# Kernel tuning notes

Hardware: AMD Instinct MI355X
Metric: run time of the kernel (lower is better)

## Reference

```python
import math
import jax, jax.numpy as jnp
import numpy as np

B, T, C, H, E, K = 2, 2048, 1024, 16, 8, 2
HID = 4 * C
D = C // H

def new_gelu(x):
    return 0.5 * x * (1.0 + jnp.tanh(math.sqrt(2.0 / math.pi) * (x + 0.044715 * x ** 3)))

def layer_norm(x, g, b, eps=1e-5):
    mu = jnp.mean(x, axis=-1, keepdims=True)
    var = jnp.var(x, axis=-1, keepdims=True)
    return (x - mu) / jnp.sqrt(var + eps) * g + b

def setup_inputs():
    key = jax.random.key(0)
    ks = jax.random.split(key, 8)
    s = 0.02
    return {
        'x': jax.random.normal(ks[0], (B, T, C), jnp.float32),
        'ln1_g': jnp.ones((C,), jnp.float32), 'ln1_b': jnp.zeros((C,), jnp.float32),
        'ln2_g': jnp.ones((C,), jnp.float32), 'ln2_b': jnp.zeros((C,), jnp.float32),
        'attn_w': (jax.random.normal(ks[1], (C, 3 * C), jnp.float32) * s),
        'attn_b': jnp.zeros((3 * C,), jnp.float32),
        'proj_w': (jax.random.normal(ks[2], (C, C), jnp.float32) * s),
        'proj_b': jnp.zeros((C,), jnp.float32),
        'router_w': (jax.random.normal(ks[3], (C, E), jnp.float32) * s),
        'fc_w': (jax.random.normal(ks[4], (E, C, HID), jnp.float32) * s),
        'fc_b': jnp.zeros((E, HID), jnp.float32),
        'pj_w': (jax.random.normal(ks[5], (E, HID, C), jnp.float32) * s),
        'pj_b': jnp.zeros((E, C), jnp.float32),
    }

def reference(x, ln1_g, ln1_b, ln2_g, ln2_b, attn_w, attn_b, proj_w, proj_b, router_w, fc_w, fc_b, pj_w, pj_b):
    # --- causal self-attention with residual ---
    h = layer_norm(x, ln1_g, ln1_b)
    qkv = h @ attn_w + attn_b                              # [B,T,3C]
    q, k, v = jnp.split(qkv, 3, axis=-1)
    q = q.reshape(B, T, H, D).transpose(0, 2, 1, 3)        # [B,H,T,D]
    k = k.reshape(B, T, H, D).transpose(0, 2, 1, 3)
    v = v.reshape(B, T, H, D).transpose(0, 2, 1, 3)
    att = jnp.einsum('bhqd,bhkd->bhqk', q, k) * (1.0 / math.sqrt(D))
    mask = jnp.tril(jnp.ones((T, T), dtype=bool))
    att = jnp.where(mask, att, jnp.float32(-jnp.inf))
    att = jax.nn.softmax(att, axis=-1)                     # dropout p=0 (eval)
    y = jnp.einsum('bhqk,bhkd->bhqd', att, v)
    y = y.transpose(0, 2, 1, 3).reshape(B, T, C)
    x = x + (y @ proj_w + proj_b)
    # --- MoE FFN with residual ---
    h2 = layer_norm(x, ln2_g, ln2_b).reshape(B * T, C)     # [N,C]
    logits = h2 @ router_w                                 # [N,E]
    probs = jax.nn.softmax(logits, axis=-1)
    topk_p, topk_i = jax.lax.top_k(probs, K)               # [N,K]
    topk_p = topk_p / jnp.sum(topk_p, axis=-1, keepdims=True)
    # dense combine weights: zero outside selected experts (same math as scatter)
    gate = jnp.zeros((B * T, E), h2.dtype).at[jnp.arange(B * T)[:, None], topk_i].add(topk_p)
    out = jnp.zeros_like(h2)
    for e in range(E):  # fixed small expert loop
        he = new_gelu(h2 @ fc_w[e] + fc_b[e])              # [N,HID]
        out = out + gate[:, e:e + 1] * (he @ pj_w[e] + pj_b[e])
    return x + out.reshape(B, T, C)
```

## Files before the change

kernel.cpp:

```cpp
#include <hip/hip_runtime.h>
#include <math.h>


typedef __bf16 b16v8 __attribute__((ext_vector_type(8)));
typedef float f32x4 __attribute__((ext_vector_type(4)));

#define MFMA(a, b, c) __builtin_amdgcn_mfma_f32_16x16x32_bf16(a, b, c, 0, 0, 0)

#define GLOAD_LDS16(g, l)                                          \
  __builtin_amdgcn_global_load_lds(                                \
      (const __attribute__((address_space(1))) void*)(g),          \
      (__attribute__((address_space(3))) void*)(l), 16, 0, 0)

constexpr int Bc = 2, Tc = 2048, Cc = 1024, Hc = 16, Dc = 64;
constexpr int Nc = Bc * Tc;
constexpr int HIDc = 4096;
constexpr int Ec = 8;
constexpr int NPAIR = Nc * 2;
constexpr int NRBMAX = NPAIR / 128 + Ec;
constexpr float LOG2E = 1.4426950408889634f;

__device__ inline unsigned short f32_bf16(float f) {
  union { float f; unsigned u; } x; x.f = f;
  unsigned r = x.u + 0x7fffu + ((x.u >> 16) & 1u);
  return (unsigned short)(r >> 16);
}

__device__ inline float gelu_f(float x) {
  float t = 2.3021188f * x * (1.f + 0.044715f * x * x);
  float e = __builtin_amdgcn_exp2f(-t);
  return x * __builtin_amdgcn_rcpf(1.f + e);
}

__device__ inline int swz(int row, int g) {
  return row * 64 + ((g ^ (row & 7)) * 8);
}

__global__ __launch_bounds__(256) void convT_kernel(
    const float* __restrict__ src, unsigned short* __restrict__ dst,
    int K, int N) {
  const size_t sb = (size_t)blockIdx.z * K * N;
  const int n0 = blockIdx.x * 32, k0 = blockIdx.y * 32;
  __shared__ float t[32][33];
  const int tx = threadIdx.x & 31, ty = threadIdx.x >> 5;
#pragma unroll
  for (int j = 0; j < 4; ++j)
    t[ty + j * 8][tx] = src[sb + (size_t)(k0 + ty + j * 8) * N + n0 + tx];
  __syncthreads();
#pragma unroll
  for (int j = 0; j < 4; ++j)
    dst[sb + (size_t)(n0 + ty + j * 8) * K + k0 + tx] = f32_bf16(t[tx][ty + j * 8]);
}

__global__ __launch_bounds__(256) void ln1_kernel(
    const float* __restrict__ x, const float* __restrict__ g,
    const float* __restrict__ b, unsigned short* __restrict__ out) {
  const int row = blockIdx.x;
  const int tid = threadIdx.x;
  const float* xr = x + (size_t)row * Cc;
  float v[4]; float s = 0.f, q = 0.f;
#pragma unroll
  for (int j = 0; j < 4; ++j) { v[j] = xr[tid + j * 256]; s += v[j]; q += v[j] * v[j]; }
#pragma unroll
  for (int m = 1; m <= 32; m <<= 1) { s += __shfl_xor(s, m); q += __shfl_xor(q, m); }
  __shared__ float red[2][4];
  const int w = tid >> 6;
  if ((tid & 63) == 0) { red[0][w] = s; red[1][w] = q; }
  __syncthreads();
  s = red[0][0] + red[0][1] + red[0][2] + red[0][3];
  q = red[1][0] + red[1][1] + red[1][2] + red[1][3];
  const float mean = s * (1.f / Cc);
  const float var = q * (1.f / Cc) - mean * mean;
  const float rstd = rsqrtf(var + 1e-5f);
#pragma unroll
  for (int j = 0; j < 4; ++j) {
    int c = tid + j * 256;
    out[(size_t)row * Cc + c] = f32_bf16((v[j] - mean) * rstd * g[c] + b[c]);
  }
}

__global__ __launch_bounds__(256) void ln2_router_kernel(
    const float* __restrict__ x, const float* __restrict__ g,
    const float* __restrict__ b, const float* __restrict__ rw,
    unsigned short* __restrict__ out, int* __restrict__ tki, float* __restrict__ tkp) {
  const int row = blockIdx.x;
  const int tid = threadIdx.x;
  const float* xr = x + (size_t)row * Cc;
  float v[4]; float s = 0.f, q = 0.f;
#pragma unroll
  for (int j = 0; j < 4; ++j) { v[j] = xr[tid + j * 256]; s += v[j]; q += v[j] * v[j]; }
#pragma unroll
  for (int m = 1; m <= 32; m <<= 1) { s += __shfl_xor(s, m); q += __shfl_xor(q, m); }
  __shared__ float red[2][4];
  const int w = tid >> 6;
  if ((tid & 63) == 0) { red[0][w] = s; red[1][w] = q; }
  __syncthreads();
  s = red[0][0] + red[0][1] + red[0][2] + red[0][3];
  q = red[1][0] + red[1][1] + red[1][2] + red[1][3];
  const float mean = s * (1.f / Cc);
  const float var = q * (1.f / Cc) - mean * mean;
  const float rstd = rsqrtf(var + 1e-5f);
  float lg[8] = {0.f, 0.f, 0.f, 0.f, 0.f, 0.f, 0.f, 0.f};
#pragma unroll
  for (int j = 0; j < 4; ++j) {
    int c = tid + j * 256;
    float nv = (v[j] - mean) * rstd * g[c] + b[c];
    out[(size_t)row * Cc + c] = f32_bf16(nv);
    const float* rwc = rw + c * 8;
#pragma unroll
    for (int e = 0; e < 8; ++e) lg[e] += nv * rwc[e];
  }
#pragma unroll
  for (int m = 1; m <= 32; m <<= 1) {
#pragma unroll
    for (int e = 0; e < 8; ++e) lg[e] += __shfl_xor(lg[e], m);
  }
  __shared__ float rl[4][8];
  if ((tid & 63) == 0) {
#pragma unroll
    for (int e = 0; e < 8; ++e) rl[w][e] = lg[e];
  }
  __syncthreads();
  if (tid == 0) {
    float L[8];
#pragma unroll
    for (int e = 0; e < 8; ++e) L[e] = rl[0][e] + rl[1][e] + rl[2][e] + rl[3][e];
    int i1 = 0;
    for (int e = 1; e < 8; ++e) if (L[e] > L[i1]) i1 = e;
    int i2 = (i1 == 0) ? 1 : 0;
    for (int e = 0; e < 8; ++e) if (e != i1 && L[e] > L[i2]) i2 = e;
    float e2 = expf(L[i2] - L[i1]);
    float inv = 1.f / (1.f + e2);
    tki[row * 2] = i1; tki[row * 2 + 1] = i2;
    tkp[row * 2] = inv; tkp[row * 2 + 1] = e2 * inv;
  }
}

__global__ __launch_bounds__(256) void count_kernel(
    const int* __restrict__ tki, int* __restrict__ counts) {
  int n = blockIdx.x * 256 + threadIdx.x;
  if (n >= Nc) return;
  atomicAdd(&counts[tki[n * 2]], 1);
  atomicAdd(&counts[tki[n * 2 + 1]], 1);
}

__global__ void scan_kernel(const int* __restrict__ counts,
                            int* __restrict__ eoff, int* __restrict__ cursor,
                            int* __restrict__ tbl_e, int* __restrict__ tbl_r0,
                            int* __restrict__ tbl_n) {
  if (threadIdx.x == 0 && blockIdx.x == 0) {
    int s = 0, nb = 0;
    for (int e = 0; e < Ec; ++e) {
      eoff[e] = s; cursor[e] = s;
      for (int r = 0; r < counts[e]; r += 128) {
        tbl_e[nb] = e; tbl_r0[nb] = r; ++nb;
      }
      s += counts[e];
    }
    eoff[Ec] = s;
    *tbl_n = nb;
  }
}

__global__ __launch_bounds__(256) void assign_kernel(
    const int* __restrict__ tki, int* __restrict__ cursor,
    int* __restrict__ slot_tok, int* __restrict__ tok2slot) {
  int n = blockIdx.x * 256 + threadIdx.x;
  if (n >= Nc) return;
#pragma unroll
  for (int kk = 0; kk < 2; ++kk) {
    int e = tki[n * 2 + kk];
    int slot = atomicAdd(&cursor[e], 1);
    slot_tok[slot] = n;
    tok2slot[n * 2 + kk] = slot;
  }
}

struct GArgs {
  const unsigned short* A;
  const unsigned short* Bt;
  const float* bias;
  int M, N, K, lda, ldb, klen;
  size_t Bstride; int biasStride;
  const int* eoff;
  const int* slot_tok;
  const int* tbl_e;
  const int* tbl_r0;
  const int* tbl_n;
  float* outF;
  const float* resid;
  unsigned short* outB;
  unsigned short* outK;
  unsigned short* outV;
};

template <int MODE>
__global__ __launch_bounds__(256) void gemm128b(GArgs g) {
  int e = 0, s0 = 0, Meff = g.M, row0;
  if constexpr (MODE == 2 || MODE == 3) {
    if ((int)blockIdx.y >= *g.tbl_n) return;
    e = g.tbl_e[blockIdx.y];
    row0 = g.tbl_r0[blockIdx.y];
    s0 = g.eoff[e];
    Meff = g.eoff[e + 1] - s0;
  } else {
    row0 = blockIdx.y * 128;
  }
  const int kh = (MODE == 3) ? blockIdx.z : 0;
  const int col0 = blockIdx.x * 128;
  const int kbase = kh * g.klen;

  __shared__ __align__(16) unsigned short As[128 * 64];
  __shared__ __align__(16) unsigned short Bs[128 * 64];

  const int tid = threadIdx.x;
  const int lane = tid & 63, w = tid >> 6;
  const int wr = w >> 1, wc = w & 1;
  const int fr = lane & 15, fg = lane >> 4;

  const unsigned short* Bt = g.Bt + (size_t)e * g.Bstride;
  const float* bias = g.bias + (size_t)e * g.biasStride;

  size_t aaddr[4], baddr[4];
#pragma unroll
  for (int i = 0; i < 4; ++i) {
    int pos = i * 256 + tid;
    int r = pos >> 3;
    int c8 = ((pos & 7) ^ (r & 7)) * 8;
    int gr = row0 + r;
    if (gr >= Meff) gr = Meff - 1;
    int srcrow;
    if constexpr (MODE == 2) srcrow = g.slot_tok[s0 + gr];
    else if constexpr (MODE == 3) srcrow = s0 + gr;
    else srcrow = gr;
    aaddr[i] = (size_t)srcrow * g.lda + kbase + c8;
    baddr[i] = (size_t)(col0 + r) * g.ldb + kbase + c8;
  }

  auto STAGE = [&](int k0) {
#pragma unroll
    for (int i = 0; i < 4; ++i) {
      GLOAD_LDS16(g.A + aaddr[i] + k0, &As[i * 2048 + w * 512]);
      GLOAD_LDS16(Bt + baddr[i] + k0, &Bs[i * 2048 + w * 512]);
    }
  };

  f32x4 acc[4][4] = {};
  const int nt = g.klen / 64;

  for (int t = 0; t < nt; ++t) {
    if (t) __syncthreads();
    STAGE(t * 64);
    __syncthreads();
    b16v8 af[4][2], bf_[4][2];
#pragma unroll
    for (int mi = 0; mi < 4; ++mi) {
      const int ar = wr * 64 + mi * 16 + fr;
      af[mi][0] = *(const b16v8*)&As[swz(ar, fg)];
      af[mi][1] = *(const b16v8*)&As[swz(ar, 4 + fg)];
    }
#pragma unroll
    for (int ni = 0; ni < 4; ++ni) {
      const int br = wc * 64 + ni * 16 + fr;
      bf_[ni][0] = *(const b16v8*)&Bs[swz(br, fg)];
      bf_[ni][1] = *(const b16v8*)&Bs[swz(br, 4 + fg)];
    }
#pragma unroll
    for (int mi = 0; mi < 4; ++mi)
#pragma unroll
      for (int ni = 0; ni < 4; ++ni) {
        acc[mi][ni] = MFMA(af[mi][0], bf_[ni][0], acc[mi][ni]);
        acc[mi][ni] = MFMA(af[mi][1], bf_[ni][1], acc[mi][ni]);
      }
  }

  float* outF3 = nullptr;
  if constexpr (MODE == 3) outF3 = g.outF + (size_t)kh * NPAIR * Cc;

#pragma unroll
  for (int mi = 0; mi < 4; ++mi) {
#pragma unroll
    for (int ni = 0; ni < 4; ++ni) {
#pragma unroll
      for (int rr = 0; rr < 4; ++rr) {
        int row = row0 + wr * 64 + mi * 16 + fg * 4 + rr;
        int col = col0 + wc * 64 + ni * 16 + fr;
        if (row >= Meff) continue;
        float bval = bias[col];
        if constexpr (MODE == 3) { if (kh != 0) bval = 0.f; }
        float val = acc[mi][ni][rr] + bval;
        if constexpr (MODE == 0) {
          int bb = row >> 11, tt = row & (Tc - 1);
          int which = col >> 10, cj = col & (Cc - 1);
          int hd = cj >> 6, d = cj & 63;
          if (which == 0)
            g.outB[(((size_t)(bb * Hc + hd)) * Tc + tt) * Dc + d] = f32_bf16(val);
          else if (which == 1)
            g.outK[(((size_t)(bb * Hc + hd)) * Tc + tt) * Dc + d] = f32_bf16(val);
          else
            g.outV[(((size_t)(bb * Hc + hd)) * Dc + d) * Tc + tt] = f32_bf16(val);
        } else if constexpr (MODE == 1) {
          size_t o = (size_t)row * g.N + col;
          g.outF[o] = val + g.resid[o];
        } else if constexpr (MODE == 2) {
          g.outB[(size_t)(s0 + row) * g.N + col] = f32_bf16(gelu_f(val));
        } else {
          outF3[(size_t)(s0 + row) * g.N + col] = val;
        }
      }
    }
  }
}

__global__ __launch_bounds__(512) void attn_kernel(
    const unsigned short* __restrict__ q, const unsigned short* __restrict__ k,
    const unsigned short* __restrict__ v, unsigned short* __restrict__ y) {
  const int qt = blockIdx.x, bh = blockIdx.y;
  const int qbase = qt * 128;
  __shared__ __align__(16) unsigned short ldsK[64][72];
  __shared__ __align__(16) unsigned short ldsVT[64][72];
  __shared__ __align__(16) unsigned short ldsP[8][16][72];
  const int tid = threadIdx.x, lane = tid & 63, w = tid >> 6;
  const int fr = lane & 15, fg = lane >> 4;
  const size_t base = (size_t)bh * Tc * Dc;
  const int qrow = qbase + w * 16 + fr;
  b16v8 qa0 = *(const b16v8*)(q + base + (size_t)qrow * Dc + fg * 8);
  b16v8 qa1 = *(const b16v8*)(q + base + (size_t)qrow * Dc + 32 + fg * 8);
  float m[4], lsum[4] = {0.f, 0.f, 0.f, 0.f};
#pragma unroll
  for (int r = 0; r < 4; ++r) m[r] = -3.0e38f;
  f32x4 oacc[4] = {};
  constexpr float SC = 0.125f * LOG2E;

  const int sr = tid >> 3, scb = (tid & 7) * 8;
  const int ntile = (qbase + 128) / 64;

  *(uint4*)&ldsK[sr][scb]  = *(const uint4*)(k + base + (size_t)sr * Dc + scb);
  *(uint4*)&ldsVT[sr][scb] = *(const uint4*)(v + base + (size_t)sr * Tc + scb);
  __syncthreads();

  for (int ti = 0; ti < ntile; ++ti) {
    const int kb = ti * 64;
    uint4 kreg, vreg;
    const bool more = (ti + 1 < ntile);
    if (more) {
      const int kn = kb + 64;
      kreg = *(const uint4*)(k + base + (size_t)(kn + sr) * Dc + scb);
      vreg = *(const uint4*)(v + base + (size_t)sr * Tc + kn + scb);
    }

    f32x4 s[4];
#pragma unroll
    for (int ni = 0; ni < 4; ++ni) {
      b16v8 kb0 = *(const b16v8*)&ldsK[ni * 16 + fr][fg * 8];
      b16v8 kb1 = *(const b16v8*)&ldsK[ni * 16 + fr][32 + fg * 8];
      f32x4 z = {};
      z = MFMA(qa0, kb0, z);
      z = MFMA(qa1, kb1, z);
      s[ni] = z;
    }
    const bool diag = (kb + 64 > qbase + w * 16);
#pragma unroll
    for (int ni = 0; ni < 4; ++ni) {
#pragma unroll
      for (int r = 0; r < 4; ++r) {
        float sv = s[ni][r] * SC;
        if (diag) {
          int gq = qbase + w * 16 + fg * 4 + r;
          int kv = kb + ni * 16 + fr;
          if (kv > gq) sv = -3.0e38f;
        }
        s[ni][r] = sv;
      }
    }
#pragma unroll
    for (int r = 0; r < 4; ++r) {
      float mx = fmaxf(fmaxf(s[0][r], s[1][r]), fmaxf(s[2][r], s[3][r]));
#pragma unroll
      for (int msk = 1; msk <= 8; msk <<= 1) mx = fmaxf(mx, __shfl_xor(mx, msk));
      float mnew = fmaxf(m[r], mx);
      float alpha = __builtin_amdgcn_exp2f(m[r] - mnew);
      float psum = 0.f;
#pragma unroll
      for (int ni = 0; ni < 4; ++ni) {
        float pp = __builtin_amdgcn_exp2f(s[ni][r] - mnew);
        s[ni][r] = pp;
        psum += pp;
      }
#pragma unroll
      for (int msk = 1; msk <= 8; msk <<= 1) psum += __shfl_xor(psum, msk);
      lsum[r] = lsum[r] * alpha + psum;
      m[r] = mnew;
#pragma unroll
      for (int ni = 0; ni < 4; ++ni) {
        oacc[ni][r] = oacc[ni][r] * alpha;
        ldsP[w][fg * 4 + r][ni * 16 + fr] = f32_bf16(s[ni][r]);
      }
    }
    asm volatile("s_waitcnt lgkmcnt(0)" ::: "memory");
    __builtin_amdgcn_sched_barrier(0);
    b16v8 pa0 = *(const b16v8*)&ldsP[w][fr][fg * 8];
    b16v8 pa1 = *(const b16v8*)&ldsP[w][fr][32 + fg * 8];
#pragma unroll
    for (int ni = 0; ni < 4; ++ni) {
      b16v8 vb0 = *(const b16v8*)&ldsVT[ni * 16 + fr][fg * 8];
      b16v8 vb1 = *(const b16v8*)&ldsVT[ni * 16 + fr][32 + fg * 8];
      oacc[ni] = MFMA(pa0, vb0, oacc[ni]);
      oacc[ni] = MFMA(pa1, vb1, oacc[ni]);
    }

    if (more) {
      __syncthreads();
      *(uint4*)&ldsK[sr][scb]  = kreg;
      *(uint4*)&ldsVT[sr][scb] = vreg;
      __syncthreads();
    }
  }

  const int bb = bh >> 4, hh = bh & 15;
#pragma unroll
  for (int r = 0; r < 4; ++r) {
    float rl = __builtin_amdgcn_rcpf(lsum[r]);
#pragma unroll
    for (int ni = 0; ni < 4; ++ni) {
      int t = qbase + w * 16 + fg * 4 + r;
      int d = ni * 16 + fr;
      y[((size_t)(bb * Tc + t)) * Cc + hh * Dc + d] = f32_bf16(oacc[ni][r] * rl);
    }
  }
}

__global__ __launch_bounds__(256) void combine_kernel(
    const float* __restrict__ pair, const float* __restrict__ tkp,
    const int* __restrict__ tok2slot, float* __restrict__ out) {
  const int n = blockIdx.x;
  const int c4 = threadIdx.x * 4;
  const int s0 = tok2slot[n * 2], s1 = tok2slot[n * 2 + 1];
  const float p0 = tkp[n * 2], p1 = tkp[n * 2 + 1];
  const float* pb = pair + (size_t)NPAIR * Cc;
  float4 a0 = *(const float4*)&pair[(size_t)s0 * Cc + c4];
  float4 a1 = *(const float4*)&pb[(size_t)s0 * Cc + c4];
  float4 b0 = *(const float4*)&pair[(size_t)s1 * Cc + c4];
  float4 b1 = *(const float4*)&pb[(size_t)s1 * Cc + c4];
  float4 o = *(float4*)&out[(size_t)n * Cc + c4];
  o.x += p0 * (a0.x + a1.x) + p1 * (b0.x + b1.x);
  o.y += p0 * (a0.y + a1.y) + p1 * (b0.y + b1.y);
  o.z += p0 * (a0.z + a1.z) + p1 * (b0.z + b1.z);
  o.w += p0 * (a0.w + a1.w) + p1 * (b0.w + b1.w);
  *(float4*)&out[(size_t)n * Cc + c4] = o;
}

extern "C" void kernel_launch(void* const* d_in, const int* in_sizes, int n_in,
                              void* d_out, int out_size, void* d_ws, size_t ws_size,
                              hipStream_t stream) {
  const float* x        = (const float*)d_in[0];
  const float* ln1_g    = (const float*)d_in[1];
  const float* ln1_b    = (const float*)d_in[2];
  const float* ln2_g    = (const float*)d_in[3];
  const float* ln2_b    = (const float*)d_in[4];
  const float* attn_w   = (const float*)d_in[5];
  const float* attn_b   = (const float*)d_in[6];
  const float* proj_w   = (const float*)d_in[7];
  const float* proj_b   = (const float*)d_in[8];
  const float* router_w = (const float*)d_in[9];
  const float* fc_w     = (const float*)d_in[10];
  const float* fc_b     = (const float*)d_in[11];
  const float* pj_w     = (const float*)d_in[12];
  const float* pj_b     = (const float*)d_in[13];
  float* out = (float*)d_out;

  char* ws = (char*)d_ws;
  size_t off = 0;
  auto alloc = [&](size_t bytes) -> void* {
    void* p = ws + off;
    off = (off + bytes + 255) & ~(size_t)255;
    return p;
  };
  unsigned short* attn_wT = (unsigned short*)alloc((size_t)3 * Cc * Cc * 2);
  unsigned short* proj_wT = (unsigned short*)alloc((size_t)Cc * Cc * 2);
  unsigned short* fc_wT   = (unsigned short*)alloc((size_t)Ec * HIDc * Cc * 2);
  unsigned short* pj_wT   = (unsigned short*)alloc((size_t)Ec * Cc * HIDc * 2);
  unsigned short* h    = (unsigned short*)alloc((size_t)Nc * Cc * 2);
  unsigned short* qb   = (unsigned short*)alloc((size_t)Nc * Cc * 2);
  unsigned short* kbuf = (unsigned short*)alloc((size_t)Nc * Cc * 2);
  unsigned short* vbuf = (unsigned short*)alloc((size_t)Nc * Cc * 2);
  unsigned short* ybuf = (unsigned short*)alloc((size_t)Nc * Cc * 2);
  unsigned short* he   = (unsigned short*)alloc((size_t)NPAIR * HIDc * 2);
  float* pairout = (float*)alloc((size_t)2 * NPAIR * Cc * 4);
  int*   tki     = (int*)alloc((size_t)Nc * 2 * 4);
  float* tkp     = (float*)alloc((size_t)Nc * 2 * 4);
  int*   counts  = (int*)alloc(Ec * 4);
  int*   eoff    = (int*)alloc((Ec + 1) * 4);
  int*   cursor  = (int*)alloc(Ec * 4);
  int*   slot_tok= (int*)alloc((size_t)NPAIR * 4);
  int*   tok2slot= (int*)alloc((size_t)Nc * 2 * 4);
  int*   tbl_e   = (int*)alloc(NRBMAX * 4);
  int*   tbl_r0  = (int*)alloc(NRBMAX * 4);
  int*   tbl_n   = (int*)alloc(4);
  (void)ws_size; (void)in_sizes; (void)n_in; (void)out_size;

  convT_kernel<<<dim3(3 * Cc / 32, Cc / 32, 1), 256, 0, stream>>>(attn_w, attn_wT, Cc, 3 * Cc);
  convT_kernel<<<dim3(Cc / 32, Cc / 32, 1), 256, 0, stream>>>(proj_w, proj_wT, Cc, Cc);
  convT_kernel<<<dim3(HIDc / 32, Cc / 32, Ec), 256, 0, stream>>>(fc_w, fc_wT, Cc, HIDc);
  convT_kernel<<<dim3(Cc / 32, HIDc / 32, Ec), 256, 0, stream>>>(pj_w, pj_wT, HIDc, Cc);

  ln1_kernel<<<Nc, 256, 0, stream>>>(x, ln1_g, ln1_b, h);

  {
    GArgs a = {};
    a.A = h; a.Bt = attn_wT; a.bias = attn_b;
    a.M = Nc; a.N = 3 * Cc; a.K = Cc; a.lda = Cc; a.ldb = Cc; a.klen = Cc;
    a.outB = qb; a.outK = kbuf; a.outV = vbuf;
    gemm128b<0><<<dim3(3 * Cc / 128, Nc / 128, 1), 256, 0, stream>>>(a);
  }

  attn_kernel<<<dim3(Tc / 128, Bc * Hc), 512, 0, stream>>>(qb, kbuf, vbuf, ybuf);

  {
    GArgs p = {};
    p.A = ybuf; p.Bt = proj_wT; p.bias = proj_b;
    p.M = Nc; p.N = Cc; p.K = Cc; p.lda = Cc; p.ldb = Cc; p.klen = Cc;
    p.outF = out; p.resid = x;
    gemm128b<1><<<dim3(Cc / 128, Nc / 128, 1), 256, 0, stream>>>(p);
  }

  ln2_router_kernel<<<Nc, 256, 0, stream>>>(out, ln2_g, ln2_b, router_w, h, tki, tkp);

  hipMemsetAsync(counts, 0, Ec * sizeof(int), stream);
  count_kernel<<<(Nc + 255) / 256, 256, 0, stream>>>(tki, counts);
  scan_kernel<<<1, 64, 0, stream>>>(counts, eoff, cursor, tbl_e, tbl_r0, tbl_n);
  assign_kernel<<<(Nc + 255) / 256, 256, 0, stream>>>(tki, cursor, slot_tok, tok2slot);

  {
    GArgs f = {};
    f.A = h; f.Bt = fc_wT; f.bias = fc_b;
    f.M = Nc; f.N = HIDc; f.K = Cc; f.lda = Cc; f.ldb = Cc; f.klen = Cc;
    f.Bstride = (size_t)HIDc * Cc; f.biasStride = HIDc;
    f.eoff = eoff; f.slot_tok = slot_tok;
    f.tbl_e = tbl_e; f.tbl_r0 = tbl_r0; f.tbl_n = tbl_n;
    f.outB = he;
    gemm128b<2><<<dim3(HIDc / 128, NRBMAX, 1), 256, 0, stream>>>(f);
  }

  {
    GArgs pj = {};
    pj.A = he; pj.Bt = pj_wT; pj.bias = pj_b;
    pj.M = Nc; pj.N = Cc; pj.K = HIDc; pj.lda = HIDc; pj.ldb = HIDc; pj.klen = HIDc / 2;
    pj.Bstride = (size_t)Cc * HIDc; pj.biasStride = Cc;
    pj.eoff = eoff;
    pj.tbl_e = tbl_e; pj.tbl_r0 = tbl_r0; pj.tbl_n = tbl_n;
    pj.outF = pairout;
    gemm128b<3><<<dim3(Cc / 128, NRBMAX, 2), 256, 0, stream>>>(pj);
  }

  combine_kernel<<<Nc, 256, 0, stream>>>(pairout, tkp, tok2slot, out);
}
```

Baseline: 636.8 us.

## Fuse MoE combine into projection GEMM epilogue via atomic scatter; reverse attention tile order

The expert projection GEMM now scales each result by its gate and atomically adds it into the output row of its token. This removes the large fp32 pair-output buffer and the separate combine kernel. The attention kernel also launches causal query tiles in reverse order so the longest tiles start first. The cost is many fp32 atomics in the GEMM epilogue and a nondeterministic summation order.

```diff
diff --git a/kernel.cpp b/kernel.cpp
--- a/kernel.cpp
+++ b/kernel.cpp
@@ -163,8 +163,9 @@
 }
 
 __global__ __launch_bounds__(256) void assign_kernel(
-    const int* __restrict__ tki, int* __restrict__ cursor,
-    int* __restrict__ slot_tok, int* __restrict__ tok2slot) {
+    const int* __restrict__ tki, const float* __restrict__ tkp,
+    int* __restrict__ cursor, int* __restrict__ slot_tok,
+    float* __restrict__ slot_gate) {
   int n = blockIdx.x * 256 + threadIdx.x;
   if (n >= Nc) return;
 #pragma unroll
@@ -172,7 +173,7 @@
     int e = tki[n * 2 + kk];
     int slot = atomicAdd(&cursor[e], 1);
     slot_tok[slot] = n;
-    tok2slot[n * 2 + kk] = slot;
+    slot_gate[slot] = tkp[n * 2 + kk];
   }
 }
 
@@ -184,6 +185,7 @@
   size_t Bstride; int biasStride;
   const int* eoff;
   const int* slot_tok;
+  const float* slot_gate;
   const int* tbl_e;
   const int* tbl_r0;
   const int* tbl_n;
@@ -273,9 +275,6 @@
         acc[mi][ni] = MFMA(af[mi][1], bf_[ni][1], acc[mi][ni]);
       }
   }
-
-  float* outF3 = nullptr;
-  if constexpr (MODE == 3) outF3 = g.outF + (size_t)kh * NPAIR * Cc;
 
 #pragma unroll
   for (int mi = 0; mi < 4; ++mi) {
@@ -305,7 +304,9 @@
         } else if constexpr (MODE == 2) {
           g.outB[(size_t)(s0 + row) * g.N + col] = f32_bf16(gelu_f(val));
         } else {
-          outF3[(size_t)(s0 + row) * g.N + col] = val;
+          int tok = g.slot_tok[s0 + row];
+          atomicAdd(&g.outF[(size_t)tok * Cc + col],
+                    g.slot_gate[s0 + row] * val);
         }
       }
     }
@@ -315,7 +316,8 @@
 __global__ __launch_bounds__(512) void attn_kernel(
     const unsigned short* __restrict__ q, const unsigned short* __restrict__ k,
     const unsigned short* __restrict__ v, unsigned short* __restrict__ y) {
-  const int qt = blockIdx.x, bh = blockIdx.y;
+  const int qt = gridDim.x - 1 - blockIdx.x;
+  const int bh = blockIdx.y;
   const int qbase = qt * 128;
   __shared__ __align__(16) unsigned short ldsK[64][72];
   __shared__ __align__(16) unsigned short ldsVT[64][72];
@@ -428,26 +430,6 @@
       y[((size_t)(bb * Tc + t)) * Cc + hh * Dc + d] = f32_bf16(oacc[ni][r] * rl);
     }
   }
-}
-
-__global__ __launch_bounds__(256) void combine_kernel(
-    const float* __restrict__ pair, const float* __restrict__ tkp,
-    const int* __restrict__ tok2slot, float* __restrict__ out) {
-  const int n = blockIdx.x;
-  const int c4 = threadIdx.x * 4;
-  const int s0 = tok2slot[n * 2], s1 = tok2slot[n * 2 + 1];
-  const float p0 = tkp[n * 2], p1 = tkp[n * 2 + 1];
-  const float* pb = pair + (size_t)NPAIR * Cc;
-  float4 a0 = *(const float4*)&pair[(size_t)s0 * Cc + c4];
-  float4 a1 = *(const float4*)&pb[(size_t)s0 * Cc + c4];
-  float4 b0 = *(const float4*)&pair[(size_t)s1 * Cc + c4];
-  float4 b1 = *(const float4*)&pb[(size_t)s1 * Cc + c4];
-  float4 o = *(float4*)&out[(size_t)n * Cc + c4];
-  o.x += p0 * (a0.x + a1.x) + p1 * (b0.x + b1.x);
-  o.y += p0 * (a0.y + a1.y) + p1 * (b0.y + b1.y);
-  o.z += p0 * (a0.z + a1.z) + p1 * (b0.z + b1.z);
-  o.w += p0 * (a0.w + a1.w) + p1 * (b0.w + b1.w);
-  *(float4*)&out[(size_t)n * Cc + c4] = o;
 }
 
 extern "C" void kernel_launch(void* const* d_in, const int* in_sizes, int n_in,
@@ -486,17 +468,16 @@
   unsigned short* vbuf = (unsigned short*)alloc((size_t)Nc * Cc * 2);
   unsigned short* ybuf = (unsigned short*)alloc((size_t)Nc * Cc * 2);
   unsigned short* he   = (unsigned short*)alloc((size_t)NPAIR * HIDc * 2);
-  float* pairout = (float*)alloc((size_t)2 * NPAIR * Cc * 4);
-  int*   tki     = (int*)alloc((size_t)Nc * 2 * 4);
-  float* tkp     = (float*)alloc((size_t)Nc * 2 * 4);
-  int*   counts  = (int*)alloc(Ec * 4);
-  int*   eoff    = (int*)alloc((Ec + 1) * 4);
-  int*   cursor  = (int*)alloc(Ec * 4);
-  int*   slot_tok= (int*)alloc((size_t)NPAIR * 4);
-  int*   tok2slot= (int*)alloc((size_t)Nc * 2 * 4);
-  int*   tbl_e   = (int*)alloc(NRBMAX * 4);
-  int*   tbl_r0  = (int*)alloc(NRBMAX * 4);
-  int*   tbl_n   = (int*)alloc(4);
+  int*   tki      = (int*)alloc((size_t)Nc * 2 * 4);
+  float* tkp      = (float*)alloc((size_t)Nc * 2 * 4);
+  int*   counts   = (int*)alloc(Ec * 4);
+  int*   eoff     = (int*)alloc((Ec + 1) * 4);
+  int*   cursor   = (int*)alloc(Ec * 4);
+  int*   slot_tok = (int*)alloc((size_t)NPAIR * 4);
+  float* slot_gate= (float*)alloc((size_t)NPAIR * 4);
+  int*   tbl_e    = (int*)alloc(NRBMAX * 4);
+  int*   tbl_r0   = (int*)alloc(NRBMAX * 4);
+  int*   tbl_n    = (int*)alloc(4);
   (void)ws_size; (void)in_sizes; (void)n_in; (void)out_size;
 
   convT_kernel<<<dim3(3 * Cc / 32, Cc / 32, 1), 256, 0, stream>>>(attn_w, attn_wT, Cc, 3 * Cc);
@@ -529,7 +510,7 @@
   hipMemsetAsync(counts, 0, Ec * sizeof(int), stream);
   count_kernel<<<(Nc + 255) / 256, 256, 0, stream>>>(tki, counts);
   scan_kernel<<<1, 64, 0, stream>>>(counts, eoff, cursor, tbl_e, tbl_r0, tbl_n);
-  assign_kernel<<<(Nc + 255) / 256, 256, 0, stream>>>(tki, cursor, slot_tok, tok2slot);
+  assign_kernel<<<(Nc + 255) / 256, 256, 0, stream>>>(tki, tkp, cursor, slot_tok, slot_gate);
 
   {
     GArgs f = {};
@@ -547,11 +528,9 @@
     pj.A = he; pj.Bt = pj_wT; pj.bias = pj_b;
     pj.M = Nc; pj.N = Cc; pj.K = HIDc; pj.lda = HIDc; pj.ldb = HIDc; pj.klen = HIDc / 2;
     pj.Bstride = (size_t)Cc * HIDc; pj.biasStride = Cc;
-    pj.eoff = eoff;
+    pj.eoff = eoff; pj.slot_tok = slot_tok; pj.slot_gate = slot_gate;
     pj.tbl_e = tbl_e; pj.tbl_r0 = tbl_r0; pj.tbl_n = tbl_n;
-    pj.outF = pairout;
+    pj.outF = out;
     gemm128b<3><<<dim3(Cc / 128, NRBMAX, 2), 256, 0, stream>>>(pj);
   }
-
-  combine_kernel<<<Nc, 256, 0, stream>>>(pairout, tkp, tok2slot, out);
-}
+}
```

Result: slower. 673.0 us (+5.7%).
